# Performance work log

Measured on AMD Instinct MI355X. Metric: run time of the kernel, lower is better.

## Reference

```python
import jax, jax.numpy as jnp
from jax import lax
import numpy as np

B, Q, T, C = 64, 900, 100, 92
W_CLASS, W_BBOX, W_GIOU = 1.0, 1.0, 1.0


def to_corners(b):
    cx, cy, w, h = b[..., 0], b[..., 1], b[..., 2], b[..., 3]
    return jnp.stack([cx - 0.5 * w, cy - 0.5 * h, cx + 0.5 * w, cy + 0.5 * h], axis=-1)


def generalized_iou(b1, b2):
    # b1 [Q,4], b2 [T,4] in corner format -> pairwise GIoU [Q,T]
    a1 = (b1[:, 2] - b1[:, 0]) * (b1[:, 3] - b1[:, 1])
    a2 = (b2[:, 2] - b2[:, 0]) * (b2[:, 3] - b2[:, 1])
    lt = jnp.maximum(b1[:, None, :2], b2[None, :, :2])
    rb = jnp.minimum(b1[:, None, 2:], b2[None, :, 2:])
    wh = jnp.clip(rb - lt, 0.0)
    inter = wh[..., 0] * wh[..., 1]
    union = a1[:, None] + a2[None, :] - inter
    iou = inter / union
    lt_e = jnp.minimum(b1[:, None, :2], b2[None, :, :2])
    rb_e = jnp.maximum(b1[:, None, 2:], b2[None, :, 2:])
    wh_e = jnp.clip(rb_e - lt_e, 0.0)
    area_e = wh_e[..., 0] * wh_e[..., 1]
    return iou - (area_e - union) / area_e


def cost_matrix(logits, pred_bbox, tgt_labels, tgt_bbox):
    conf = jax.nn.softmax(logits, axis=-1)                                  # [B,Q,C]
    cost_class = -jax.vmap(lambda c, l: c[:, l])(conf, tgt_labels)          # [B,Q,T]
    cost_bbox = jnp.sum(jnp.abs(pred_bbox[:, :, None, :] - tgt_bbox[:, None, :, :]), axis=-1)
    cost_giou = -jax.vmap(generalized_iou)(to_corners(pred_bbox), to_corners(tgt_bbox))
    return W_BBOX * cost_bbox + W_CLASS * cost_class + W_GIOU * cost_giou   # [B,Q,T]


def solve_lsa(cost):
    # Jonker-Volgenant shortest-augmenting-path optimal assignment.
    # cost [n, m] with n <= m; assigns every row to a distinct column.
    n, m = cost.shape
    INF = jnp.asarray(1e9, cost.dtype)

    def assign_row(i, carry):
        u, v, p = carry        # u [n+1], v [m+1] potentials; p [m+1]: row assigned to col (0=free)
        p = p.at[0].set(i + 1)
        minv0 = jnp.full(m + 1, INF, cost.dtype)
        used0 = jnp.zeros(m + 1, bool)
        way0 = jnp.zeros(m + 1, jnp.int32)

        def cond(s):
            j0, u, v, p, minv, used, way = s
            return p[j0] != 0

        def body(s):
            j0, u, v, p, minv, used, way = s
            used = used.at[j0].set(True)
            i0 = p[j0]
            cur = cost[i0 - 1] - u[i0] - v[1:]          # reduced costs over cols 1..m
            cur = jnp.where(used[1:], INF, cur)
            better = cur < minv[1:]
            minv = minv.at[1:].set(jnp.where(better, cur, minv[1:]))
            way = way.at[1:].set(jnp.where(better, j0, way[1:]))
            masked = jnp.where(used[1:], INF, minv[1:])
            j1 = jnp.argmin(masked).astype(jnp.int32) + 1
            delta = masked[j1 - 1]
            u = u.at[p].add(jnp.where(used, delta, jnp.zeros((), cost.dtype)))
            v = v - jnp.where(used, delta, jnp.zeros((), cost.dtype))
            minv = minv - jnp.where(used, jnp.zeros((), cost.dtype), delta)
            return j1, u, v, p, minv, used, way

        j0, u, v, p, _, _, way = lax.while_loop(
            cond, body, (jnp.int32(0), u, v, p, minv0, used0, way0))

        def aug_cond(s):
            jj, p = s
            return jj != 0

        def aug_body(s):
            jj, p = s
            j1 = way[jj]
            p = p.at[jj].set(p[j1])
            return j1, p

        _, p = lax.while_loop(aug_cond, aug_body, (j0, p))
        return u, v, p

    u0 = jnp.zeros(n + 1, cost.dtype)
    v0 = jnp.zeros(m + 1, cost.dtype)
    p0 = jnp.zeros(m + 1, jnp.int32)
    _, _, p = lax.fori_loop(0, n, assign_row, (u0, v0, p0))
    # column (0-based) assigned to each row i
    q = jnp.argmax(p[1:, None] == (jnp.arange(n, dtype=jnp.int32) + 1)[None, :], axis=0)
    order = jnp.argsort(q)
    return q[order].astype(jnp.int32), order.astype(jnp.int32)


def setup_inputs() -> dict:
    key = jax.random.key(0)
    k1, k2, k3, k4 = jax.random.split(key, 4)
    return {
        'logits': jax.random.normal(k1, (B, Q, C), jnp.float32),
        'pred_bbox': jax.random.uniform(k2, (B, Q, 4), jnp.float32),
        'tgt_labels': jax.random.randint(k3, (B, T), 0, C, jnp.int32),
        'tgt_bbox': jax.random.uniform(k4, (B, T, 4), jnp.float32),
    }


def reference(logits, pred_bbox, tgt_labels, tgt_bbox):
    cost = cost_matrix(logits, pred_bbox, tgt_labels, tgt_bbox)   # [B,Q,T]
    # scipy solves the [Q,T] problem (Q > T): transpose so rows (targets) <= cols (queries).
    row_ind, col_ind = jax.vmap(lambda c: solve_lsa(c.T))(cost)
    # row_ind: query indices (ascending), col_ind: matched target indices, per image.
    return cost, row_ind, col_ind
```

## Files before the change

kernel.cpp:

```cpp
#include <hip/hip_runtime.h>
#include <cmath>

#define Bq 64
#define Qn 900
#define Tn 100
#define Cn 92
#define INFN 1e9f
#define QT 64
#define NQT 15

__device__ inline unsigned fkey(float x) {
    unsigned u = __float_as_uint(x);
    return (u & 0x80000000u) ? ~u : (u | 0x80000000u);
}
__device__ inline float unfkey(unsigned k) {
    unsigned u = (k & 0x80000000u) ? (k & 0x7FFFFFFFu) : ~k;
    return __uint_as_float(u);
}

__device__ inline unsigned wave_min_u32(unsigned x) {
    unsigned t;
#define DPPSTEP(ctrl)                                                          \
    t = (unsigned)__builtin_amdgcn_update_dpp((int)0xFFFFFFFF, (int)x, ctrl,   \
                                              0xF, 0xF, false);                \
    x = (t < x) ? t : x;
    DPPSTEP(0x111)
    DPPSTEP(0x112)
    DPPSTEP(0x114)
    DPPSTEP(0x118)
    DPPSTEP(0x142)
    DPPSTEP(0x143)
#undef DPPSTEP
    return (unsigned)__builtin_amdgcn_readlane((int)x, 63);
}

__global__ __launch_bounds__(256) void cost_fused_kernel(
        const float* __restrict__ logits,
        const float* __restrict__ pred_bbox,
        const int*   __restrict__ tgt_labels,
        const float* __restrict__ tgt_bbox,
        float* __restrict__ cost,
        float* __restrict__ costT,
        unsigned long long* __restrict__ tilemin)
{
    const int b   = blockIdx.y;
    const int q0  = blockIdx.x * QT;
    const int nq  = (q0 + QT <= Qn) ? QT : (Qn - q0);
    const int tid = threadIdx.x;

    __shared__ float prob[QT * Cn];
    __shared__ float pb_s[QT][4];
    __shared__ float tb_s[Tn][4];
    __shared__ int   lab_s[Tn];
    __shared__ float ctile[QT][Tn + 1];

    const float* lg_src = logits + ((size_t)b * Qn + q0) * Cn;
    for (int idx = tid; idx < nq * Cn; idx += 256) prob[idx] = lg_src[idx];
    for (int idx = tid; idx < nq * 4; idx += 256)
        ((float*)pb_s)[idx] = pred_bbox[((size_t)b * Qn + q0) * 4 + idx];
    for (int idx = tid; idx < Tn * 4; idx += 256)
        ((float*)tb_s)[idx] = tgt_bbox[(size_t)b * Tn * 4 + idx];
    for (int idx = tid; idx < Tn; idx += 256)
        lab_s[idx] = tgt_labels[b * Tn + idx];
    __syncthreads();

    const int g = tid >> 2, l4 = tid & 3;
    if (g < nq) {
        float mx = -3.0e38f;
        for (int c = l4; c < Cn; c += 4) mx = fmaxf(mx, prob[g * Cn + c]);
        mx = fmaxf(mx, __shfl_xor(mx, 1));
        mx = fmaxf(mx, __shfl_xor(mx, 2));
        float s = 0.0f;
        for (int c = l4; c < Cn; c += 4) {
            float e = expf(prob[g * Cn + c] - mx);
            prob[g * Cn + c] = e;
            s += e;
        }
        s += __shfl_xor(s, 1);
        s += __shfl_xor(s, 2);
        float inv = 1.0f / s;
        for (int c = l4; c < Cn; c += 4) prob[g * Cn + c] *= inv;
    }
    __syncthreads();

    const int total = nq * Tn;
    float* cdst = cost + (size_t)b * Qn * Tn + (size_t)q0 * Tn;
    for (int flat = tid; flat < total; flat += 256) {
        int q = flat / Tn, tt = flat - q * Tn;
        float pcx = pb_s[q][0], pcy = pb_s[q][1], pw = pb_s[q][2], ph = pb_s[q][3];
        float tcx = tb_s[tt][0], tcy = tb_s[tt][1], tw = tb_s[tt][2], th = tb_s[tt][3];

        float cclass = -prob[q * Cn + lab_s[tt]];
        float cbbox  = fabsf(pcx - tcx) + fabsf(pcy - tcy)
                     + fabsf(pw - tw)  + fabsf(ph - th);

        float px1 = pcx - 0.5f * pw, py1 = pcy - 0.5f * ph;
        float px2 = pcx + 0.5f * pw, py2 = pcy + 0.5f * ph;
        float tx1 = tcx - 0.5f * tw, ty1 = tcy - 0.5f * th;
        float tx2 = tcx + 0.5f * tw, ty2 = tcy + 0.5f * th;

        float a1 = (px2 - px1) * (py2 - py1);
        float a2 = (tx2 - tx1) * (ty2 - ty1);
        float iw = fmaxf(fminf(px2, tx2) - fmaxf(px1, tx1), 0.0f);
        float ih = fmaxf(fminf(py2, ty2) - fmaxf(py1, ty1), 0.0f);
        float inter = iw * ih;
        float uni = a1 + a2 - inter;
        float iou = inter / uni;
        float ew = fmaxf(fmaxf(px2, tx2) - fminf(px1, tx1), 0.0f);
        float eh = fmaxf(fmaxf(py2, ty2) - fminf(py1, ty1), 0.0f);
        float ae = ew * eh;
        float val = cbbox + cclass - (iou - (ae - uni) / ae);

        cdst[flat] = val;
        ctile[q][tt] = val;
    }
    __syncthreads();

    if (costT) {
        float* tdst = costT + (size_t)b * Qn * Tn + q0;
        if (nq == QT) {
            for (int flat = tid; flat < QT * Tn; flat += 256) {
                int r = flat >> 6, c = flat & 63;
                tdst[(size_t)r * Qn + c] = ctile[c][r];
            }
        } else {
            for (int flat = tid; flat < nq * Tn; flat += 256) {
                int r = flat / nq, c = flat - r * nq;
                tdst[(size_t)r * Qn + c] = ctile[c][r];
            }
        }
    }
    if (tilemin && tid < Tn) {
        float bvv = 3.0e38f; int bq = 0;
        for (int q = 0; q < nq; ++q) {
            float x = ctile[q][tid];
            if (x < bvv) { bvv = x; bq = q; }
        }
        tilemin[((size_t)b * NQT + blockIdx.x) * Tn + tid] =
            ((unsigned long long)fkey(bvv) << 32) | (unsigned)(q0 + bq);
    }
}

template<bool TM>
__global__ __launch_bounds__(256) void jv_kernel(
        const float* __restrict__ costT,
        const unsigned long long* __restrict__ tilemin,
        float* __restrict__ out)
{
    const int b    = blockIdx.x;
    const int tid  = threadIdx.x;
    const int lane = tid & 63;
    const int wv   = tid >> 6;

    __shared__ int   p0_lds[1024];
    __shared__ int   way_lds[1024];
    __shared__ float u_lds[Tn + 1];
    __shared__ int   amin_lds[Tn];
    __shared__ unsigned char asg[Tn];
    __shared__ int   freelist[Tn];
    __shared__ int   nfree_s;
    __shared__ int   qarr[Tn];

    for (int j = tid; j < 1024; j += 256) p0_lds[j] = 0;
    if (tid == 0) nfree_s = 0;
    __syncthreads();

    const float* cb = costT + (size_t)b * Qn * Tn;

    if (TM) {
        if (tid < Tn) {
            unsigned long long best = ~0ull;
            for (int t = 0; t < NQT; ++t) {
                unsigned long long v = tilemin[((size_t)b * NQT + t) * Tn + tid];
                if (v < best) best = v;
            }
            u_lds[tid + 1] = unfkey((unsigned)(best >> 32));
            amin_lds[tid]  = (int)(best & 0xFFFFFFFFu);
        }
    } else {
        for (int r = wv; r < Tn; r += 4) {
            float bv = 3.0e38f; int bj = 0x3fffffff;
            #pragma unroll
            for (int k = 0; k < 15; ++k) {
                int c = lane + 64 * k;
                if (c < Qn) {
                    float x = cb[(size_t)r * Qn + c];
                    if (x < bv) { bv = x; bj = c; }
                }
            }
            #pragma unroll
            for (int off = 1; off < 64; off <<= 1) {
                float ov = __shfl_xor(bv, off);
                int   oj = __shfl_xor(bj, off);
                if (ov < bv || (ov == bv && oj < bj)) { bv = ov; bj = oj; }
            }
            if (lane == 0) { u_lds[r + 1] = bv; amin_lds[r] = bj; }
        }
    }
    __syncthreads();

    if (tid < Tn) {
        int j = amin_lds[tid];
        int old = atomicCAS(&p0_lds[j], 0, tid + 1);
        asg[tid] = (old == 0) ? 1 : 0;
    }
    __syncthreads();
    if (tid < Tn && !asg[tid]) {
        int s = atomicAdd(&nfree_s, 1);
        freelist[s] = tid;
    }
    __syncthreads();
    const int nfree = nfree_s;

    if (wv == 0 && nfree > 0) {
        const int cbase = lane << 4;
        float v_r[16], dist_r[16], rc[16];
        int   p_r[16];
        #pragma unroll
        for (int k = 0; k < 16; ++k) v_r[k] = 0.0f;

#define LOADROW(dst, row1)                                                     \
        {                                                                      \
            const float* rp = cb + (size_t)((row1) - 1) * Qn;                  \
            if (cbase + 16 <= Qn) {                                            \
                _Pragma("unroll")                                              \
                for (int w4 = 0; w4 < 4; ++w4) {                               \
                    float4 f = *(const float4*)(rp + cbase + 4 * w4);          \
                    dst[4*w4+0] = f.x; dst[4*w4+1] = f.y;                      \
                    dst[4*w4+2] = f.z; dst[4*w4+3] = f.w;                      \
                }                                                              \
            } else {                                                           \
                _Pragma("unroll")                                              \
                for (int k = 0; k < 16; ++k)                                   \
                    dst[k] = (cbase + k < Qn) ? rp[cbase + k] : 3.0e38f;       \
            }                                                                  \
        }

        for (int s = 0; s < nfree; ++s) {
            const int ri = freelist[s];

            {
                const int4* pp = (const int4*)(p0_lds + cbase);
                int4 a = pp[0], bb = pp[1], cc4 = pp[2], dd4 = pp[3];
                p_r[0]=a.x;  p_r[1]=a.y;  p_r[2]=a.z;  p_r[3]=a.w;
                p_r[4]=bb.x; p_r[5]=bb.y; p_r[6]=bb.z; p_r[7]=bb.w;
                p_r[8]=cc4.x; p_r[9]=cc4.y; p_r[10]=cc4.z; p_r[11]=cc4.w;
                p_r[12]=dd4.x; p_r[13]=dd4.y; p_r[14]=dd4.z; p_r[15]=dd4.w;
            }
            #pragma unroll
            for (int k = 0; k < 16; ++k) dist_r[k] = 3.0e38f;
            unsigned um = 0;
            int   i0   = ri + 1;
            float d0   = 0.0f;
            int   jenc = 0;
            int   sink0 = -1;
            float dstar = 0.0f;

            LOADROW(rc, i0);
            float ui0 = u_lds[i0];

            for (int it = 0; it < Tn + 2; ++it) {
                const float sft = d0 - ui0;
                float bv = 3.0e38f; int bj = 0x7fffffff; int bown = 0;
                #pragma unroll
                for (int k = 0; k < 16; ++k) {
                    int c = cbase + k;
                    if (c < Qn && !((um >> k) & 1u)) {
                        float cand = sft + rc[k] - v_r[k];
                        if (cand < dist_r[k]) {
                            dist_r[k] = cand;
                            way_lds[(k << 6) | lane] = jenc;
                        }
                        if (dist_r[k] < bv) { bv = dist_r[k]; bj = c; bown = p_r[k]; }
                    }
                }
                unsigned tk = fkey(bv);
                unsigned gk = wave_min_u32(tk);
                unsigned long long msk = __ballot(tk == gk);
                int src = __ffsll(msk) - 1;
                int   bestj = __shfl(bj, src);
                float delta = __shfl(bv, src);
                int   bp    = __shfl(bown, src);

                if (bp == 0) { sink0 = bestj; dstar = delta; break; }

                if ((bestj >> 4) == lane) um |= 1u << (bestj & 15);
                LOADROW(rc, bp);
                ui0 = u_lds[bp];
                d0 = delta; i0 = bp; jenc = bestj + 1;
            }

            if (lane == 0) u_lds[ri + 1] += dstar;
            #pragma unroll
            for (int k = 0; k < 16; ++k) {
                if ((um >> k) & 1u) {
                    float dd = dstar - dist_r[k];
                    v_r[k] -= dd;
                    u_lds[p_r[k]] += dd;
                }
            }

            if (lane == 0 && sink0 >= 0) {
                int jj = sink0;
                while (true) {
                    int w = way_lds[((jj & 15) << 6) | (jj >> 4)];
                    if (w == 0) { p0_lds[jj] = ri + 1; break; }
                    p0_lds[jj] = p0_lds[w - 1];
                    jj = w - 1;
                }
            }
        }
#undef LOADROW
    }
    __syncthreads();

    for (int c = tid; c < Qn; c += 256) {
        int r = p0_lds[c];
        if (r) qarr[r - 1] = c;
    }
    __syncthreads();

    float* out_row = out + (size_t)Bq * Qn * Tn + (size_t)b * Tn;
    float* out_col = out_row + (size_t)Bq * Tn;
    for (int i = tid; i < Tn; i += 256) {
        int qi = qarr[i];
        int rank = 0;
        for (int jj = 0; jj < Tn; ++jj) rank += (qarr[jj] < qi) ? 1 : 0;
        out_row[rank] = (float)qi;
        out_col[rank] = (float)i;
    }
}

__global__ __launch_bounds__(256) void jv_compat_kernel(
        const float* __restrict__ cost,
        float* __restrict__ out)
{
    const int b    = blockIdx.x;
    const int tid  = threadIdx.x;
    const int lane = tid & 63;
    const int wv   = tid >> 6;
    const bool act = (tid < Qn / 4);

    __shared__ int   p_lds[Qn + 1];
    __shared__ int   way_lds[Qn + 1];
    __shared__ float u_lds[Tn + 1];
    __shared__ int   amin_lds[Tn];
    __shared__ unsigned char asg[Tn];
    __shared__ int   freelist[Tn];
    __shared__ int   nfree_s;
    __shared__ float redv[2][4];
    __shared__ int   redj[2][4];
    __shared__ int   qarr[Tn];

    for (int j = tid; j <= Qn; j += 256) p_lds[j] = 0;
    if (tid == 0) nfree_s = 0;
    __syncthreads();

    const float* cb = cost + (size_t)b * Qn * Tn;

    for (int r = wv; r < Tn; r += 4) {
        float bv = 3.0e38f; int bj = 0x3fffffff;
        #pragma unroll
        for (int k = 0; k < 15; ++k) {
            int c = lane + 64 * k;
            if (c < Qn) {
                float x = cb[(size_t)c * Tn + r];
                if (x < bv) { bv = x; bj = c; }
            }
        }
        #pragma unroll
        for (int off = 1; off < 64; off <<= 1) {
            float ov = __shfl_xor(bv, off);
            int   oj = __shfl_xor(bj, off);
            if (ov < bv || (ov == bv && oj < bj)) { bv = ov; bj = oj; }
        }
        if (lane == 0) { u_lds[r + 1] = bv; amin_lds[r] = bj; }
    }
    __syncthreads();

    if (tid < Tn) {
        int j = amin_lds[tid];
        int old = atomicCAS(&p_lds[j + 1], 0, tid + 1);
        asg[tid] = (old == 0) ? 1 : 0;
    }
    __syncthreads();
    if (tid < Tn && !asg[tid]) {
        int s = atomicAdd(&nfree_s, 1);
        freelist[s] = tid;
    }
    __syncthreads();
    const int nfree = nfree_s;

    const int cbase = 4 * tid;
    float varr[4] = {0.0f, 0.0f, 0.0f, 0.0f};

    for (int s = 0; s < nfree; ++s) {
        const int ri = freelist[s];
        float minv[4] = {INFN, INFN, INFN, INFN};
        unsigned um = 0;
        int i0 = ri + 1, j0 = 0;
        if (tid == 0) p_lds[0] = i0;

        float c0v = 0, c1v = 0, c2v = 0, c3v = 0;
        if (act) {
            const float* cp = cb + (i0 - 1);
            c0v = cp[(size_t)cbase * Tn];       c1v = cp[(size_t)(cbase + 1) * Tn];
            c2v = cp[(size_t)(cbase + 2) * Tn]; c3v = cp[(size_t)(cbase + 3) * Tn];
        }
        float ui0 = u_lds[i0];

        for (int it = 0; it < Tn + 2; ++it) {
            if (j0 > 0 && act) {
                int cc = j0 - 1;
                if ((cc >> 2) == tid) um |= 1u << (cc & 3);
            }
            float bv = 3.0e9f; int bj = 0x3fffffff;
            if (act) {
                float crr[4] = {c0v, c1v, c2v, c3v};
                #pragma unroll
                for (int k = 0; k < 4; ++k) {
                    if (!((um >> k) & 1u)) {
                        float cur = crr[k] - ui0 - varr[k];
                        if (cur < minv[k]) { minv[k] = cur; way_lds[cbase + k + 1] = j0; }
                        if (minv[k] < bv) { bv = minv[k]; bj = cbase + k + 1; }
                    }
                }
            }
            #pragma unroll
            for (int off = 1; off < 64; off <<= 1) {
                float ov = __shfl_xor(bv, off);
                int   oj = __shfl_xor(bj, off);
                if (ov < bv || (ov == bv && oj < bj)) { bv = ov; bj = oj; }
            }
            const int par = it & 1;
            if (lane == 0) { redv[par][wv] = bv; redj[par][wv] = bj; }
            __syncthreads();
            float delta = redv[par][0]; int bestj = redj[par][0];
            #pragma unroll
            for (int w = 1; w < 4; ++w) {
                float ov = redv[par][w]; int oj = redj[par][w];
                if (ov < delta || (ov == delta && oj < bestj)) { delta = ov; bestj = oj; }
            }
            const int bp = p_lds[bestj];

            float ui_n = 0.0f, n0 = 0, n1 = 0, n2 = 0, n3 = 0;
            if (bp != 0) {
                if (act) {
                    const float* cp = cb + (bp - 1);
                    n0 = cp[(size_t)cbase * Tn];       n1 = cp[(size_t)(cbase + 1) * Tn];
                    n2 = cp[(size_t)(cbase + 2) * Tn]; n3 = cp[(size_t)(cbase + 3) * Tn];
                }
                ui_n = u_lds[bp];
            }

            if (tid == 0) u_lds[ri + 1] += delta;
            if (act) {
                #pragma unroll
                for (int k = 0; k < 4; ++k) {
                    if ((um >> k) & 1u) {
                        varr[k] -= delta;
                        u_lds[p_lds[cbase + k + 1]] += delta;
                    } else {
                        minv[k] -= delta;
                    }
                }
            }
            j0 = bestj;
            if (bp == 0) break;
            i0 = bp; ui0 = ui_n;
            c0v = n0; c1v = n1; c2v = n2; c3v = n3;
        }

        if (tid == 0) {
            int jj = j0;
            while (jj != 0) { int j1 = way_lds[jj]; p_lds[jj] = p_lds[j1]; jj = j1; }
        }
        __syncthreads();
    }

    for (int j = tid + 1; j <= Qn; j += 256) {
        int r = p_lds[j];
        if (r) qarr[r - 1] = j - 1;
    }
    __syncthreads();

    float* out_row = out + (size_t)Bq * Qn * Tn + (size_t)b * Tn;
    float* out_col = out_row + (size_t)Bq * Tn;
    for (int i = tid; i < Tn; i += 256) {
        int qi = qarr[i];
        int rank = 0;
        for (int jj = 0; jj < Tn; ++jj) rank += (qarr[jj] < qi) ? 1 : 0;
        out_row[rank] = (float)qi;
        out_col[rank] = (float)i;
    }
}

extern "C" void kernel_launch(void* const* d_in, const int* in_sizes, int n_in,
                              void* d_out, int out_size, void* d_ws, size_t ws_size,
                              hipStream_t stream) {
    const float* logits     = (const float*)d_in[0];
    const float* pred_bbox  = (const float*)d_in[1];
    const int*   tgt_labels = (const int*)d_in[2];
    const float* tgt_bbox   = (const float*)d_in[3];
    float* out = (float*)d_out;

    const size_t needT  = (size_t)Bq * Qn * Tn * sizeof(float);
    const size_t needTM = needT + (size_t)Bq * NQT * Tn * 8 + 4096;

    if (ws_size >= needTM) {
        float* costT = (float*)d_ws;
        unsigned long long* tilemin = (unsigned long long*)((char*)d_ws + needT);
        hipLaunchKernelGGL(cost_fused_kernel, dim3(NQT, Bq), dim3(256), 0, stream,
                           logits, pred_bbox, tgt_labels, tgt_bbox, out, costT, tilemin);
        hipLaunchKernelGGL((jv_kernel<true>), dim3(Bq), dim3(256), 0, stream,
                           costT, tilemin, out);
    } else if (ws_size >= needT) {
        float* costT = (float*)d_ws;
        hipLaunchKernelGGL(cost_fused_kernel, dim3(NQT, Bq), dim3(256), 0, stream,
                           logits, pred_bbox, tgt_labels, tgt_bbox, out, costT,
                           (unsigned long long*)nullptr);
        hipLaunchKernelGGL((jv_kernel<false>), dim3(Bq), dim3(256), 0, stream,
                           costT, (const unsigned long long*)nullptr, out);
    } else {
        hipLaunchKernelGGL(cost_fused_kernel, dim3(NQT, Bq), dim3(256), 0, stream,
                           logits, pred_bbox, tgt_labels, tgt_bbox, out,
                           (float*)nullptr, (unsigned long long*)nullptr);
        hipLaunchKernelGGL(jv_compat_kernel, dim3(Bq), dim3(256), 0, stream,
                           out, out);
    }
}
```

Measured before the change: 103.8 us.

## Add two auction-style augmenting row reduction passes before shortest-path augmentation

```diff
diff --git a/kernel.cpp b/kernel.cpp
--- a/kernel.cpp
+++ b/kernel.cpp
@@ -158,6 +158,7 @@
     __shared__ int   amin_lds[Tn];
     __shared__ unsigned char asg[Tn];
     __shared__ int   freelist[Tn];
+    __shared__ int   fl2[Tn];
     __shared__ int   nfree_s;
     __shared__ int   qarr[Tn];
 
@@ -236,7 +237,53 @@
             }                                                                  \
         }
 
-        for (int s = 0; s < nfree; ++s) {
+        int cnt = nfree;
+        #pragma unroll 1
+        for (int pass = 0; pass < 2; ++pass) {
+            int cnt_out = 0;
+            #pragma unroll 1
+            for (int s = 0; s < cnt; ++s) {
+                const int i = (pass == 0) ? freelist[s] : fl2[s];
+                LOADROW(rc, i + 1);
+
+                float m1 = 3.0e38f, m2 = 3.0e38f; int j1 = 0x7fffffff;
+                #pragma unroll
+                for (int k = 0; k < 16; ++k) {
+                    int c = cbase + k;
+                    if (c < Qn) {
+                        float cur = rc[k] - v_r[k];
+                        if (cur < m1) { m2 = m1; m1 = cur; j1 = c; }
+                        else if (cur < m2) { m2 = cur; }
+                    }
+                }
+                #pragma unroll
+                for (int off = 1; off < 64; off <<= 1) {
+                    float om1 = __shfl_xor(m1, off), om2 = __shfl_xor(m2, off);
+                    int   oj1 = __shfl_xor(j1, off);
+                    if (om1 < m1 || (om1 == m1 && oj1 < j1)) {
+                        m2 = fminf(m1, om2);
+                        m1 = om1; j1 = oj1;
+                    } else {
+                        m2 = fminf(m2, om1);
+                    }
+                }
+                if (lane == 0) u_lds[i + 1] = m2;
+                if ((j1 >> 4) == lane) v_r[j1 & 15] -= (m2 - m1);
+                const int kown = p0_lds[j1];
+                if (lane == 0) p0_lds[j1] = i + 1;
+                if (kown != 0) {
+                    if (lane == 0) {
+                        if (pass == 0) fl2[cnt_out] = kown - 1;
+                        else           freelist[cnt_out] = kown - 1;
+                    }
+                    cnt_out++;
+                }
+            }
+            cnt = cnt_out;
+        }
+
+        #pragma unroll 1
+        for (int s = 0; s < cnt; ++s) {
             const int ri = freelist[s];
 
             {
@@ -309,6 +356,7 @@
                     jj = w - 1;
                 }
             }
+            __threadfence_block();
         }
 #undef LOADROW
     }
```

After: 126.9 us. +22.2%, slower.
